# Kernel tuning notes

Hardware: AMD Instinct MI355X
Metric: run time of the kernel (lower is better)

Reference implementation:

```python
import jax, jax.numpy as jnp
import numpy as np

N, E, C, NE, G, T = 20000, 320000, 32, 10, 64, 1000
NB, HID, LAYERS = 8, 64, 2
R_MAX, P_CUT, AVG_NEIGH = 5.0, 6, 16.0
LM = 16  # (max_ell+1)^2 spherical-harmonic components
L_OF_LM = jnp.array([0,1,1,1,2,2,2,2,2,3,3,3,3,3,3,3])


def sph_harm(u):
    # component-normalized real spherical harmonics up to l=3 on unit vectors u [E,3]
    x, y, z = u[:, 0], u[:, 1], u[:, 2]
    s3, s15, s5, s105, s7 = 3**0.5, 15**0.5, 5**0.5, 105**0.5, 7**0.5
    s35_8, s21_8 = (35.0/8.0)**0.5, (21.0/8.0)**0.5
    comps = [jnp.ones_like(x),
             s3*x, s3*y, s3*z,
             s15*x*y, s15*y*z, 0.5*s5*(3*z*z-1.0), s15*x*z, 0.5*s15*(x*x-y*y),
             s35_8*y*(3*x*x-y*y), s105*x*y*z, s21_8*y*(5*z*z-1.0),
             0.5*s7*(5*z*z*z-3*z), s21_8*x*(5*z*z-1.0),
             0.5*s105*z*(x*x-y*y), s35_8*x*(x*x-3*y*y)]
    return jnp.stack(comps, axis=-1)  # [E,16]


def radial_embed(r):
    # Bessel basis with polynomial cutoff (MACE RadialEmbeddingBlock)
    n = jnp.arange(1, NB + 1, dtype=r.dtype)
    rc = jnp.maximum(r, 1e-9)
    bessel = (2.0/R_MAX)**0.5 * jnp.sin(n[None, :]*jnp.pi*rc[:, None]/R_MAX) / rc[:, None]
    xr = r / R_MAX
    p = float(P_CUT)
    f = (1.0 - 0.5*(p+1)*(p+2)*xr**p + p*(p+2)*xr**(p+1) - 0.5*p*(p+1)*xr**(p+2))
    f = f * (xr < 1.0)
    return bessel * f[:, None]  # [E,NB]


def setup_inputs():
    key = jax.random.key(0)
    ks = jax.random.split(key, 16)
    positions = jax.random.normal(ks[0], (N, 3)) * 3.0
    species = jax.random.randint(ks[1], (N,), 0, NE)
    node_attrs = jax.nn.one_hot(species, NE, dtype=jnp.float32)
    edge_index = jax.random.randint(ks[2], (2, E), 0, N)
    shifts = jnp.zeros((E, 3), jnp.float32)
    batch = jnp.sort(jax.random.randint(ks[3], (N,), 0, G))
    t = jax.random.randint(ks[4], (G,), 0, T)
    eps = jax.random.normal(ks[5], (N, NE + 3))
    betas = jnp.linspace(1e-4, 0.02, T)
    alpha_bar = jnp.cumprod(1.0 - betas)
    sc = 0.1
    W_embed = sc * jax.random.normal(ks[6], (NE + 1, C))
    W_r1 = sc * jax.random.normal(ks[7], (LAYERS, NB, HID))
    W_r2 = sc * jax.random.normal(ks[8], (LAYERS, HID, C * 4))
    W_mix = sc * jax.random.normal(ks[9], (LAYERS, 4, C, C))
    W_sc = sc * jax.random.normal(ks[10], (NE, C))
    W_prod = sc * jax.random.normal(ks[11], (LAYERS, 3, C))
    W_ro_s = sc * jax.random.normal(ks[12], (LAYERS, C, NE))
    W_ro_v = sc * jax.random.normal(ks[13], (LAYERS, C))
    return {"positions": positions, "node_attrs": node_attrs, "shifts": shifts,
            "eps": eps, "alpha_bar": alpha_bar, "W_embed": W_embed, "W_r1": W_r1,
            "W_r2": W_r2, "W_mix": W_mix, "W_sc": W_sc, "W_prod": W_prod,
            "W_ro_s": W_ro_s, "W_ro_v": W_ro_v, "edge_index": edge_index,
            "batch": batch, "t": t}


def reference(positions, node_attrs, shifts, eps, alpha_bar, W_embed, W_r1, W_r2,
              W_mix, W_sc, W_prod, W_ro_s, W_ro_v, edge_index, batch, t):
    sender, receiver = edge_index[0], edge_index[1]
    # diffusion: noise positions and attrs (DDPM q(x_t|x_0))
    ab = alpha_bar[t][batch][:, None]                       # [N,1]
    attrs0 = node_attrs / 4.0
    pos_noisy = jnp.sqrt(ab) * positions + jnp.sqrt(1.0 - ab) * eps[:, -3:]
    attrs_noisy = jnp.sqrt(ab) * attrs0 + jnp.sqrt(1.0 - ab) * eps[:, :NE]
    tf = (t.astype(jnp.float32) / T)[batch][:, None]
    h = jnp.concatenate([attrs_noisy, tf], axis=-1) @ W_embed  # [N,C]
    # edge geometry
    vec = pos_noisy[receiver] - pos_noisy[sender] + shifts
    r = jnp.sqrt(jnp.sum(vec * vec, axis=-1) + 1e-12)
    Y = sph_harm(vec / r[:, None])                          # [E,16]
    ef = radial_embed(r)                                    # [E,NB]
    scalar = h
    pred = jnp.zeros((N, NE + 3), h.dtype)
    for layer in range(LAYERS):
        rw = jax.nn.silu(ef @ W_r1[layer]) @ W_r2[layer]    # [E,4C]
        rw = rw.reshape(E, C, 4)[:, :, L_OF_LM]             # [E,C,16]
        msg = rw * scalar[sender][:, :, None] * Y[:, None, :]
        agg = jax.ops.segment_sum(msg, receiver, num_segments=N) / AVG_NEIGH
        Wm = W_mix[layer][L_OF_LM]                          # [16,C,C]
        feats = jnp.einsum('nck,kcd->ndk', agg, Wm)         # per-l channel mix
        s = feats[:, :, 0]
        poly = W_prod[layer, 0] + W_prod[layer, 1] * s + W_prod[layer, 2] * s * s
        feats = feats * poly[:, :, None]                    # correlation-3 product
        if layer == 0:
            feats = feats.at[:, :, 0].add(attrs_noisy @ W_sc)  # element skip
        scalar = feats[:, :, 0]
        pred_s = scalar @ W_ro_s[layer]                     # [N,NE]
        pred_v = jnp.einsum('ncm,c->nm', feats[:, :, 1:4], W_ro_v[layer])  # [N,3]
        pred = pred + jnp.concatenate([pred_s, pred_v], axis=-1)
    err = (pred - eps) ** 2
    loss_pos = jax.ops.segment_sum(err[:, -3:].sum(-1), batch, num_segments=G)
    loss_lab = jax.ops.segment_sum(err[:, :NE].sum(-1), batch, num_segments=G)
    nn = jax.ops.segment_sum(jnp.ones((N,), pred.dtype), batch, num_segments=G)
    loss = 0.5 * (loss_pos + loss_lab) / (jnp.maximum(nn, 1.0) * (3 + NE))
    return loss
```

## Files before the change

### kernel.cpp

```cpp
#include <hip/hip_runtime.h>

typedef unsigned short ushort_t;
typedef unsigned int uint_t;

#define NN 20000
#define EE 320000
#define CC 32
#define NEL 10
#define GG 64
#define TTT 1000
#define NBB 8
#define HIDD 64
#define EPB 256

typedef __attribute__((ext_vector_type(8))) short bf16x8;
typedef __attribute__((ext_vector_type(4))) float f32x4;

__device__ __forceinline__ float bits2f(uint_t b) { union { uint_t u; float f; } v; v.u = b; return v.f; }
__device__ __forceinline__ ushort_t f2b(float f) {
  union { float f; uint_t u; } v; v.f = f;
  uint_t r = (v.u + 0x7fffu + ((v.u >> 16) & 1u)) >> 16;
  return (ushort_t)r;
}
__device__ __forceinline__ uint_t pk(float a, float b) {
  return (uint_t)f2b(a) | ((uint_t)f2b(b) << 16);
}
__device__ __forceinline__ float lo16(uint_t u) { return bits2f(u << 16); }
__device__ __forceinline__ float hi16(uint_t u) { return bits2f(u & 0xffff0000u); }

__global__ __launch_bounds__(256) void k_prep(
    const float* __restrict__ positions, const float* __restrict__ node_attrs,
    const float* __restrict__ eps, const float* __restrict__ alpha_bar,
    const float* __restrict__ W_embed, const float* __restrict__ W_sc,
    const int* __restrict__ batch, const int* __restrict__ tarr,
    float* __restrict__ pos_noisy, float* __restrict__ scalA,
    float* __restrict__ sc_skip, float* __restrict__ pred, int* __restrict__ deg)
{
  int n = blockIdx.x * 256 + threadIdx.x;
  if (n >= NN) return;
  deg[n] = 0;
  int g = batch[n];
  int tn = tarr[g];
  float ab = alpha_bar[tn];
  float sa = sqrtf(ab), sb = sqrtf(fmaxf(1.0f - ab, 0.0f));
#pragma unroll
  for (int j = 0; j < 3; ++j)
    pos_noisy[n * 3 + j] = sa * positions[n * 3 + j] + sb * eps[n * 13 + 10 + j];
  float an[10];
#pragma unroll
  for (int j = 0; j < 10; ++j)
    an[j] = sa * 0.25f * node_attrs[n * 10 + j] + sb * eps[n * 13 + j];
  float tf = (float)tn * (1.0f / (float)TTT);
  for (int d = 0; d < CC; ++d) {
    float h = tf * W_embed[10 * CC + d];
    float sk = 0.0f;
#pragma unroll
    for (int j = 0; j < 10; ++j) {
      h = fmaf(an[j], W_embed[j * CC + d], h);
      sk = fmaf(an[j], W_sc[j * CC + d], sk);
    }
    scalA[n * CC + d] = h;
    sc_skip[n * CC + d] = sk;
  }
#pragma unroll
  for (int j = 0; j < 13; ++j) pred[n * 13 + j] = 0.0f;
}

__global__ __launch_bounds__(256) void k_edge_deg(const int* __restrict__ ei,
    int* __restrict__ deg)
{
  int e = blockIdx.x * 256 + threadIdx.x;
  atomicAdd(&deg[ei[EE + e]], 1);
}

__global__ __launch_bounds__(1024) void k_scan(const int* __restrict__ deg,
    int* __restrict__ offs, int* __restrict__ cursor,
    float* __restrict__ lnum, float* __restrict__ lcnt)
{
  __shared__ int wsums[16];
  __shared__ int woffs[16];
  int tid = threadIdx.x, lane = tid & 63, wv = tid >> 6;
  if (tid < GG) { lnum[tid] = 0.0f; lcnt[tid] = 0.0f; }
  int base = tid * 20;
  int loc[20];
  int s = 0;
#pragma unroll
  for (int j = 0; j < 20; ++j) {
    int idx = base + j;
    int v = (idx < NN) ? deg[idx] : 0;
    loc[j] = s; s += v;
  }
  int inc = s;
  for (int o = 1; o < 64; o <<= 1) {
    int v = __shfl_up(inc, o, 64);
    if (lane >= o) inc += v;
  }
  if (lane == 63) wsums[wv] = inc;
  __syncthreads();
  if (wv == 0 && lane < 16) {
    int v = wsums[lane];
    int i2 = v;
    for (int o = 1; o < 16; o <<= 1) {
      int vv = __shfl_up(i2, o, 16);
      if (lane >= o) i2 += vv;
    }
    woffs[lane] = i2 - v;
  }
  __syncthreads();
  int texcl = woffs[wv] + (inc - s);
#pragma unroll
  for (int j = 0; j < 20; ++j) {
    int idx = base + j;
    if (idx < NN) { int v = texcl + loc[j]; offs[idx] = v; cursor[idx] = v; }
  }
  if (tid == 1023) offs[NN] = EE;
}

__global__ __launch_bounds__(256) void k_edge2(
    const float* __restrict__ pos_noisy, const float* __restrict__ shifts,
    const int* __restrict__ ei, int* __restrict__ cursor,
    ushort_t* __restrict__ Ys, ushort_t* __restrict__ efs, int* __restrict__ snds)
{
  int e = blockIdx.x * 256 + threadIdx.x;
  int snd = ei[e], rcv = ei[EE + e];
  float vx = pos_noisy[rcv * 3 + 0] - pos_noisy[snd * 3 + 0] + shifts[e * 3 + 0];
  float vy = pos_noisy[rcv * 3 + 1] - pos_noisy[snd * 3 + 1] + shifts[e * 3 + 1];
  float vz = pos_noisy[rcv * 3 + 2] - pos_noisy[snd * 3 + 2] + shifts[e * 3 + 2];
  float r2 = vx * vx + vy * vy + vz * vz + 1e-12f;
  float r = sqrtf(r2);
  float inv = 1.0f / r;
  float x = vx * inv, y = vy * inv, z = vz * inv;

  const float s3 = 1.7320508075688772f, s15 = 3.872983346207417f, s5 = 2.23606797749979f;
  const float s105 = 10.246950765959598f, s7 = 2.6457513110645907f;
  const float s35_8 = 2.091650066335189f, s21_8 = 1.6201851746019651f;
  float yv[16];
  yv[0] = 1.0f;
  yv[1] = s3 * x; yv[2] = s3 * y; yv[3] = s3 * z;
  yv[4] = s15 * x * y;
  yv[5] = s15 * y * z;
  yv[6] = 0.5f * s5 * (3.0f * z * z - 1.0f);
  yv[7] = s15 * x * z;
  yv[8] = 0.5f * s15 * (x * x - y * y);
  yv[9] = s35_8 * y * (3.0f * x * x - y * y);
  yv[10] = s105 * x * y * z;
  yv[11] = s21_8 * y * (5.0f * z * z - 1.0f);
  yv[12] = 0.5f * s7 * (5.0f * z * z * z - 3.0f * z);
  yv[13] = s21_8 * x * (5.0f * z * z - 1.0f);
  yv[14] = 0.5f * s105 * z * (x * x - y * y);
  yv[15] = s35_8 * x * (x * x - 3.0f * y * y);

  float rc = fmaxf(r, 1e-9f);
  float pref = 0.6324555320336759f / rc;
  float th = 0.6283185307179586f * rc;
  float s1 = __sinf(th), c1 = __cosf(th);
  float xr = r * 0.2f;
  float fcut = 0.0f;
  if (xr < 1.0f) {
    float x2 = xr * xr, x3 = x2 * xr;
    float x6 = x3 * x3, x7 = x6 * xr, x8 = x7 * xr;
    fcut = 1.0f - 28.0f * x6 + 48.0f * x7 - 21.0f * x8;
  }
  float efv[8];
  float sp = 0.0f, scur = s1, c2 = 2.0f * c1;
#pragma unroll
  for (int b = 0; b < 8; ++b) {
    efv[b] = pref * scur * fcut;
    float nx = c2 * scur - sp;
    sp = scur; scur = nx;
  }

  int slot = atomicAdd(&cursor[rcv], 1);
  snds[slot] = snd;
  uint4* Y4 = (uint4*)Ys;
  Y4[(size_t)slot * 2 + 0] = make_uint4(pk(yv[0], yv[1]), pk(yv[2], yv[3]),
                                        pk(yv[4], yv[5]), pk(yv[6], yv[7]));
  Y4[(size_t)slot * 2 + 1] = make_uint4(pk(yv[8], yv[9]), pk(yv[10], yv[11]),
                                        pk(yv[12], yv[13]), pk(yv[14], yv[15]));
  ((uint4*)efs)[slot] = make_uint4(pk(efv[0], efv[1]), pk(efv[2], efv[3]),
                                   pk(efv[4], efv[5]), pk(efv[6], efv[7]));
}

__global__ __launch_bounds__(256) void k_rw_mfma(
    const ushort_t* __restrict__ efs, const float* __restrict__ W_r1,
    const float* __restrict__ W_r2, ushort_t* __restrict__ rwc, int layer)
{
  __shared__ __align__(16) ushort_t w2t[128][72];
  __shared__ __align__(16) ushort_t h1[EPB][72];
  int tid = threadIdx.x;
  const float* W1g = W_r1 + layer * NBB * HIDD;
  const float* W2g = W_r2 + layer * HIDD * 128;
  for (int idx = tid; idx < HIDD * 128; idx += 256) {
    int k = idx >> 7, n = idx & 127;
    w2t[n][k] = f2b(W2g[idx]);
  }
  {
    int e = blockIdx.x * EPB + tid;
    uint4 q = ((const uint4*)efs)[e];
    float efr[8] = {lo16(q.x), hi16(q.x), lo16(q.y), hi16(q.y),
                    lo16(q.z), hi16(q.z), lo16(q.w), hi16(q.w)};
    for (int hc = 0; hc < 8; ++hc) {
      float v[8];
#pragma unroll
      for (int hh = 0; hh < 8; ++hh) {
        int h = hc * 8 + hh;
        float t = 0.0f;
#pragma unroll
        for (int b = 0; b < 8; ++b) t = fmaf(efr[b], W1g[b * HIDD + h], t);
        v[hh] = t / (1.0f + __expf(-t));
      }
      *(uint4*)&h1[tid][hc * 8] = make_uint4(pk(v[0], v[1]), pk(v[2], v[3]),
                                             pk(v[4], v[5]), pk(v[6], v[7]));
    }
  }
  __syncthreads();
  int w = tid >> 6, lane = tid & 63;
  int c = lane & 15, quad = lane >> 4;
  bf16x8 bfr[16];
#pragma unroll
  for (int nt = 0; nt < 8; ++nt)
#pragma unroll
    for (int kt = 0; kt < 2; ++kt)
      bfr[nt * 2 + kt] = *(const bf16x8*)&w2t[nt * 16 + c][kt * 32 + quad * 8];
  int mb0 = w * 64;
#pragma unroll
  for (int mt = 0; mt < 4; ++mt) {
    int mbase = mb0 + mt * 16;
    bf16x8 a0 = *(const bf16x8*)&h1[mbase + c][quad * 8];
    bf16x8 a1 = *(const bf16x8*)&h1[mbase + c][32 + quad * 8];
    size_t erow = (size_t)blockIdx.x * EPB + mbase + quad * 4;
#pragma unroll
    for (int nt = 0; nt < 8; ++nt) {
      f32x4 acc = {0.0f, 0.0f, 0.0f, 0.0f};
      acc = __builtin_amdgcn_mfma_f32_16x16x32_bf16(a0, bfr[nt * 2 + 0], acc, 0, 0, 0);
      acc = __builtin_amdgcn_mfma_f32_16x16x32_bf16(a1, bfr[nt * 2 + 1], acc, 0, 0, 0);
      int col = nt * 16 + c;
#pragma unroll
      for (int r = 0; r < 4; ++r)
        rwc[(erow + r) * 128 + col] = f2b(acc[r]);
    }
  }
}

__global__ __launch_bounds__(256) void k_layer(
    const ushort_t* __restrict__ Ys, const ushort_t* __restrict__ rwc,
    const int* __restrict__ snds,
    const float* __restrict__ scal_in, float* __restrict__ scal_out,
    const int* __restrict__ offs,
    const float* __restrict__ W_mix, const float* __restrict__ W_prod,
    const float* __restrict__ W_ro_s, const float* __restrict__ W_ro_v,
    const float* __restrict__ sc_skip, float* __restrict__ pred, int layer)
{
  __shared__ float lagg[4][CC][16];
  __shared__ float lf[4][CC][4];
  int w = threadIdx.x >> 6, lane = threadIdx.x & 63;
  int n = blockIdx.x * 4 + w;
  int c = lane >> 1;
  int kh = lane & 1;
  int kb = kh * 8;
  int i0 = offs[n], i1 = offs[n + 1];
  float acc0 = 0, acc1 = 0, acc2 = 0, acc3 = 0, acc4 = 0, acc5 = 0, acc6 = 0, acc7 = 0;
  const uint4* Y4 = (const uint4*)Ys;
  const uint2* rw2 = (const uint2*)rwc;
  for (int s = i0; s < i1; ++s) {
    uint4 q = Y4[(size_t)s * 2 + kh];
    uint2 rp = rw2[(size_t)s * 32 + c];
    float ss = scal_in[snds[s] * CC + c];
    float r0 = lo16(rp.x), r1 = hi16(rp.x), r2v = lo16(rp.y), r3 = hi16(rp.y);
    float w0 = kh ? r2v : r0;
    float w13 = kh ? r3 : r1;
    float w47 = kh ? r3 : r2v;
    float ya0 = lo16(q.x), ya1 = hi16(q.x), ya2 = lo16(q.y), ya3 = hi16(q.y);
    float yb0 = lo16(q.z), yb1 = hi16(q.z), yb2 = lo16(q.w), yb3 = hi16(q.w);
    acc0 = fmaf(w0 * ss, ya0, acc0);
    acc1 = fmaf(w13 * ss, ya1, acc1);
    acc2 = fmaf(w13 * ss, ya2, acc2);
    acc3 = fmaf(w13 * ss, ya3, acc3);
    acc4 = fmaf(w47 * ss, yb0, acc4);
    acc5 = fmaf(w47 * ss, yb1, acc5);
    acc6 = fmaf(w47 * ss, yb2, acc6);
    acc7 = fmaf(w47 * ss, yb3, acc7);
  }
  const float invavg = 1.0f / 16.0f;
  lagg[w][c][kb + 0] = acc0 * invavg;
  lagg[w][c][kb + 1] = acc1 * invavg;
  lagg[w][c][kb + 2] = acc2 * invavg;
  lagg[w][c][kb + 3] = acc3 * invavg;
  lagg[w][c][kb + 4] = acc4 * invavg;
  lagg[w][c][kb + 5] = acc5 * invavg;
  lagg[w][c][kb + 6] = acc6 * invavg;
  lagg[w][c][kb + 7] = acc7 * invavg;
  __syncthreads();
  int d = c;
  float ft[8] = {0, 0, 0, 0, 0, 0, 0, 0};
  const float* Wm = W_mix + layer * 4096;
  for (int cc2 = 0; cc2 < CC; ++cc2) {
    float m0 = Wm[cc2 * CC + d];
    float m1 = Wm[1024 + cc2 * CC + d];
    float m2 = Wm[2048 + cc2 * CC + d];
    float m3 = Wm[3072 + cc2 * CC + d];
    float u0 = kh ? m2 : m0;
    float u13 = kh ? m3 : m1;
    float u47 = kh ? m3 : m2;
    ft[0] = fmaf(lagg[w][cc2][kb + 0], u0, ft[0]);
    ft[1] = fmaf(lagg[w][cc2][kb + 1], u13, ft[1]);
    ft[2] = fmaf(lagg[w][cc2][kb + 2], u13, ft[2]);
    ft[3] = fmaf(lagg[w][cc2][kb + 3], u13, ft[3]);
    ft[4] = fmaf(lagg[w][cc2][kb + 4], u47, ft[4]);
    ft[5] = fmaf(lagg[w][cc2][kb + 5], u47, ft[5]);
    ft[6] = fmaf(lagg[w][cc2][kb + 6], u47, ft[6]);
    ft[7] = fmaf(lagg[w][cc2][kb + 7], u47, ft[7]);
  }
  float s = __shfl(ft[0], lane & 62, 64);
  const float* Wp = W_prod + layer * 96;
  float p0 = Wp[d], p1 = Wp[32 + d], p2 = Wp[64 + d];
  float poly = fmaf(fmaf(p2, s, p1), s, p0);
#pragma unroll
  for (int j = 0; j < 8; ++j) ft[j] *= poly;
  if (layer == 0 && kh == 0) ft[0] += sc_skip[n * CC + d];
  if (kh == 0) {
    scal_out[n * CC + d] = ft[0];
    lf[w][d][0] = ft[0]; lf[w][d][1] = ft[1]; lf[w][d][2] = ft[2]; lf[w][d][3] = ft[3];
  }
  __syncthreads();
  if (lane < 13) {
    float sum = 0.0f;
    if (lane < 10) {
      const float* Wr = W_ro_s + layer * CC * NEL;
      for (int dd = 0; dd < CC; ++dd) sum = fmaf(lf[w][dd][0], Wr[dd * NEL + lane], sum);
    } else {
      int mm = lane - 10;
      const float* Wv = W_ro_v + layer * CC;
      for (int dd = 0; dd < CC; ++dd) sum = fmaf(lf[w][dd][1 + mm], Wv[dd], sum);
    }
    pred[n * 13 + lane] += sum;
  }
}

__global__ __launch_bounds__(256) void k_loss(const float* __restrict__ pred,
    const float* __restrict__ eps, const int* __restrict__ batch,
    float* __restrict__ lnum, float* __restrict__ lcnt)
{
  __shared__ float psum[GG];
  __shared__ int pcnt[GG];
  int tid = threadIdx.x;
  if (tid < GG) { psum[tid] = 0.0f; pcnt[tid] = 0; }
  __syncthreads();
  int n = blockIdx.x * 256 + tid;
  if (n < NN) {
    int g = batch[n];
    float sum = 0.0f;
#pragma unroll
    for (int j = 0; j < 13; ++j) {
      float dlt = pred[n * 13 + j] - eps[n * 13 + j];
      sum = fmaf(dlt, dlt, sum);
    }
    atomicAdd(&psum[g], sum);
    atomicAdd(&pcnt[g], 1);
  }
  __syncthreads();
  if (tid < GG && pcnt[tid] > 0) {
    atomicAdd(&lnum[tid], psum[tid]);
    atomicAdd(&lcnt[tid], (float)pcnt[tid]);
  }
}

__global__ void k_final(const float* __restrict__ lnum, const float* __restrict__ lcnt,
    float* __restrict__ out)
{
  int g = threadIdx.x;
  if (g < GG) {
    float nn = fmaxf(lcnt[g], 1.0f);
    out[g] = 0.5f * lnum[g] / (nn * 13.0f);
  }
}

extern "C" void kernel_launch(void* const* d_in, const int* in_sizes, int n_in,
                              void* d_out, int out_size, void* d_ws, size_t ws_size,
                              hipStream_t stream) {
  const float* positions  = (const float*)d_in[0];
  const float* node_attrs = (const float*)d_in[1];
  const float* shifts     = (const float*)d_in[2];
  const float* eps        = (const float*)d_in[3];
  const float* alpha_bar  = (const float*)d_in[4];
  const float* W_embed    = (const float*)d_in[5];
  const float* W_r1       = (const float*)d_in[6];
  const float* W_r2       = (const float*)d_in[7];
  const float* W_mix      = (const float*)d_in[8];
  const float* W_sc       = (const float*)d_in[9];
  const float* W_prod     = (const float*)d_in[10];
  const float* W_ro_s     = (const float*)d_in[11];
  const float* W_ro_v     = (const float*)d_in[12];
  const int* edge_index   = (const int*)d_in[13];
  const int* batch        = (const int*)d_in[14];
  const int* tarr         = (const int*)d_in[15];
  float* out = (float*)d_out;

  char* ws = (char*)d_ws;
  size_t off = 0;
  auto alloc = [&](size_t bytes) -> void* {
    void* p = ws + off;
    off = (off + bytes + 255) & ~(size_t)255;
    return p;
  };
  float* pos_noisy = (float*)alloc(NN * 3 * 4);
  float* scalA     = (float*)alloc(NN * CC * 4);
  float* scalB     = (float*)alloc(NN * CC * 4);
  float* sc_skip   = (float*)alloc(NN * CC * 4);
  float* pred      = (float*)alloc(NN * 13 * 4);
  ushort_t* Ys     = (ushort_t*)alloc((size_t)EE * 16 * 2);
  ushort_t* efs    = (ushort_t*)alloc((size_t)EE * 8 * 2);
  int* snds        = (int*)alloc((size_t)EE * 4);
  ushort_t* rwc    = (ushort_t*)alloc((size_t)EE * 128 * 2);
  int* deg         = (int*)alloc(NN * 4);
  int* offs        = (int*)alloc((NN + 1) * 4);
  int* cursor      = (int*)alloc(NN * 4);
  float* lnum      = (float*)alloc(GG * 4);
  float* lcnt      = (float*)alloc(GG * 4);
  (void)ws_size; (void)in_sizes; (void)n_in; (void)out_size;

  const int NB_N = (NN + 255) / 256;
  const int NB_E = EE / 256;

  k_prep<<<NB_N, 256, 0, stream>>>(positions, node_attrs, eps, alpha_bar, W_embed,
                                   W_sc, batch, tarr, pos_noisy, scalA, sc_skip, pred, deg);
  k_edge_deg<<<NB_E, 256, 0, stream>>>(edge_index, deg);
  k_scan<<<1, 1024, 0, stream>>>(deg, offs, cursor, lnum, lcnt);
  k_edge2<<<NB_E, 256, 0, stream>>>(pos_noisy, shifts, edge_index, cursor, Ys, efs, snds);

  for (int layer = 0; layer < 2; ++layer) {
    const float* sin_p = (layer == 0) ? scalA : scalB;
    float* sout_p      = (layer == 0) ? scalB : scalA;
    k_rw_mfma<<<NB_E, 256, 0, stream>>>(efs, W_r1, W_r2, rwc, layer);
    k_layer<<<NN / 4, 256, 0, stream>>>(Ys, rwc, snds, sin_p, sout_p, offs,
                                        W_mix, W_prod, W_ro_s, W_ro_v,
                                        sc_skip, pred, layer);
  }

  k_loss<<<NB_N, 256, 0, stream>>>(pred, eps, batch, lnum, lcnt);
  k_final<<<1, 64, 0, stream>>>(lnum, lcnt, out);
}
```

Baseline: 362.4 us.

## Fold sender scalar gather into radial-weight MFMA kernel; unroll edge loop by two

The multiplication by the sender node's scalar features moves out of the per-node aggregation loop and into the radial-weight MFMA epilogue, so rwc already holds the weight times the sender scalar. This removes the dependent snds load followed by the scal_in gather from the latency-bound aggregation loop, which is also unrolled by two to keep more loads in flight. In exchange the MFMA kernel now performs scattered gathers from scal_in in its epilogue, and the product is rounded to bf16 before storage, which changes precision slightly.

```diff
diff --git a/kernel.cpp b/kernel.cpp
--- a/kernel.cpp
+++ b/kernel.cpp
@@ -183,7 +183,8 @@
 
 __global__ __launch_bounds__(256) void k_rw_mfma(
     const ushort_t* __restrict__ efs, const float* __restrict__ W_r1,
-    const float* __restrict__ W_r2, ushort_t* __restrict__ rwc, int layer)
+    const float* __restrict__ W_r2, const int* __restrict__ snds,
+    const float* __restrict__ scal_in, ushort_t* __restrict__ rwc, int layer)
 {
   __shared__ __align__(16) ushort_t w2t[128][72];
   __shared__ __align__(16) ushort_t h1[EPB][72];
@@ -229,23 +230,29 @@
     bf16x8 a0 = *(const bf16x8*)&h1[mbase + c][quad * 8];
     bf16x8 a1 = *(const bf16x8*)&h1[mbase + c][32 + quad * 8];
     size_t erow = (size_t)blockIdx.x * EPB + mbase + quad * 4;
+    int4 sn = *(const int4*)&snds[erow];
+    const float* sb0 = scal_in + (size_t)sn.x * CC;
+    const float* sb1 = scal_in + (size_t)sn.y * CC;
+    const float* sb2 = scal_in + (size_t)sn.z * CC;
+    const float* sb3 = scal_in + (size_t)sn.w * CC;
 #pragma unroll
     for (int nt = 0; nt < 8; ++nt) {
       f32x4 acc = {0.0f, 0.0f, 0.0f, 0.0f};
       acc = __builtin_amdgcn_mfma_f32_16x16x32_bf16(a0, bfr[nt * 2 + 0], acc, 0, 0, 0);
       acc = __builtin_amdgcn_mfma_f32_16x16x32_bf16(a1, bfr[nt * 2 + 1], acc, 0, 0, 0);
       int col = nt * 16 + c;
-#pragma unroll
-      for (int r = 0; r < 4; ++r)
-        rwc[(erow + r) * 128 + col] = f2b(acc[r]);
+      int cc = col >> 2;
+      rwc[(erow + 0) * 128 + col] = f2b(acc[0] * sb0[cc]);
+      rwc[(erow + 1) * 128 + col] = f2b(acc[1] * sb1[cc]);
+      rwc[(erow + 2) * 128 + col] = f2b(acc[2] * sb2[cc]);
+      rwc[(erow + 3) * 128 + col] = f2b(acc[3] * sb3[cc]);
     }
   }
 }
 
 __global__ __launch_bounds__(256) void k_layer(
     const ushort_t* __restrict__ Ys, const ushort_t* __restrict__ rwc,
-    const int* __restrict__ snds,
-    const float* __restrict__ scal_in, float* __restrict__ scal_out,
+    float* __restrict__ scal_out,
     const int* __restrict__ offs,
     const float* __restrict__ W_mix, const float* __restrict__ W_prod,
     const float* __restrict__ W_ro_s, const float* __restrict__ W_ro_v,
@@ -262,24 +269,50 @@
   float acc0 = 0, acc1 = 0, acc2 = 0, acc3 = 0, acc4 = 0, acc5 = 0, acc6 = 0, acc7 = 0;
   const uint4* Y4 = (const uint4*)Ys;
   const uint2* rw2 = (const uint2*)rwc;
-  for (int s = i0; s < i1; ++s) {
+  int s = i0;
+  for (; s + 2 <= i1; s += 2) {
+    uint4 qa = Y4[(size_t)s * 2 + kh];
+    uint2 ra = rw2[(size_t)s * 32 + c];
+    uint4 qb = Y4[(size_t)(s + 1) * 2 + kh];
+    uint2 rb = rw2[(size_t)(s + 1) * 32 + c];
+    {
+      float r0 = lo16(ra.x), r1 = hi16(ra.x), r2v = lo16(ra.y), r3 = hi16(ra.y);
+      float w0 = kh ? r2v : r0, w13 = kh ? r3 : r1, w47 = kh ? r3 : r2v;
+      acc0 = fmaf(w0,  lo16(qa.x), acc0);
+      acc1 = fmaf(w13, hi16(qa.x), acc1);
+      acc2 = fmaf(w13, lo16(qa.y), acc2);
+      acc3 = fmaf(w13, hi16(qa.y), acc3);
+      acc4 = fmaf(w47, lo16(qa.z), acc4);
+      acc5 = fmaf(w47, hi16(qa.z), acc5);
+      acc6 = fmaf(w47, lo16(qa.w), acc6);
+      acc7 = fmaf(w47, hi16(qa.w), acc7);
+    }
+    {
+      float r0 = lo16(rb.x), r1 = hi16(rb.x), r2v = lo16(rb.y), r3 = hi16(rb.y);
+      float w0 = kh ? r2v : r0, w13 = kh ? r3 : r1, w47 = kh ? r3 : r2v;
+      acc0 = fmaf(w0,  lo16(qb.x), acc0);
+      acc1 = fmaf(w13, hi16(qb.x), acc1);
+      acc2 = fmaf(w13, lo16(qb.y), acc2);
+      acc3 = fmaf(w13, hi16(qb.y), acc3);
+      acc4 = fmaf(w47, lo16(qb.z), acc4);
+      acc5 = fmaf(w47, hi16(qb.z), acc5);
+      acc6 = fmaf(w47, lo16(qb.w), acc6);
+      acc7 = fmaf(w47, hi16(qb.w), acc7);
+    }
+  }
+  if (s < i1) {
     uint4 q = Y4[(size_t)s * 2 + kh];
     uint2 rp = rw2[(size_t)s * 32 + c];
-    float ss = scal_in[snds[s] * CC + c];
     float r0 = lo16(rp.x), r1 = hi16(rp.x), r2v = lo16(rp.y), r3 = hi16(rp.y);
-    float w0 = kh ? r2v : r0;
-    float w13 = kh ? r3 : r1;
-    float w47 = kh ? r3 : r2v;
-    float ya0 = lo16(q.x), ya1 = hi16(q.x), ya2 = lo16(q.y), ya3 = hi16(q.y);
-    float yb0 = lo16(q.z), yb1 = hi16(q.z), yb2 = lo16(q.w), yb3 = hi16(q.w);
-    acc0 = fmaf(w0 * ss, ya0, acc0);
-    acc1 = fmaf(w13 * ss, ya1, acc1);
-    acc2 = fmaf(w13 * ss, ya2, acc2);
-    acc3 = fmaf(w13 * ss, ya3, acc3);
-    acc4 = fmaf(w47 * ss, yb0, acc4);
-    acc5 = fmaf(w47 * ss, yb1, acc5);
-    acc6 = fmaf(w47 * ss, yb2, acc6);
-    acc7 = fmaf(w47 * ss, yb3, acc7);
+    float w0 = kh ? r2v : r0, w13 = kh ? r3 : r1, w47 = kh ? r3 : r2v;
+    acc0 = fmaf(w0,  lo16(q.x), acc0);
+    acc1 = fmaf(w13, hi16(q.x), acc1);
+    acc2 = fmaf(w13, lo16(q.y), acc2);
+    acc3 = fmaf(w13, hi16(q.y), acc3);
+    acc4 = fmaf(w47, lo16(q.z), acc4);
+    acc5 = fmaf(w47, hi16(q.z), acc5);
+    acc6 = fmaf(w47, lo16(q.w), acc6);
+    acc7 = fmaf(w47, hi16(q.w), acc7);
   }
   const float invavg = 1.0f / 16.0f;
   lagg[w][c][kb + 0] = acc0 * invavg;
@@ -311,10 +344,10 @@
     ft[6] = fmaf(lagg[w][cc2][kb + 6], u47, ft[6]);
     ft[7] = fmaf(lagg[w][cc2][kb + 7], u47, ft[7]);
   }
-  float s = __shfl(ft[0], lane & 62, 64);
+  float sv = __shfl(ft[0], lane & 62, 64);
   const float* Wp = W_prod + layer * 96;
   float p0 = Wp[d], p1 = Wp[32 + d], p2 = Wp[64 + d];
-  float poly = fmaf(fmaf(p2, s, p1), s, p0);
+  float poly = fmaf(fmaf(p2, sv, p1), sv, p0);
 #pragma unroll
   for (int j = 0; j < 8; ++j) ft[j] *= poly;
   if (layer == 0 && kh == 0) ft[0] += sc_skip[n * CC + d];
@@ -431,8 +464,8 @@
   for (int layer = 0; layer < 2; ++layer) {
     const float* sin_p = (layer == 0) ? scalA : scalB;
     float* sout_p      = (layer == 0) ? scalB : scalA;
-    k_rw_mfma<<<NB_E, 256, 0, stream>>>(efs, W_r1, W_r2, rwc, layer);
-    k_layer<<<NN / 4, 256, 0, stream>>>(Ys, rwc, snds, sin_p, sout_p, offs,
+    k_rw_mfma<<<NB_E, 256, 0, stream>>>(efs, W_r1, W_r2, snds, sin_p, rwc, layer);
+    k_layer<<<NN / 4, 256, 0, stream>>>(Ys, rwc, sout_p, offs,
                                         W_mix, W_prod, W_ro_s, W_ro_v,
                                         sc_skip, pred, layer);
   }
```

Result: faster. 341.6 us (-5.7%).

## Fuse radial MLP MFMA into per-node message aggregation kernel

Applied to the files above, without the earlier changes.

The radial-weight MFMA kernel and the per-node layer kernel are merged into one. Each block handles 4 receiver nodes: it computes the radial MLP for their edges in 16-edge tiles, multiplies by sender scalars and spherical harmonics, and reduces into shared memory with atomics. This removes the large bf16 per-edge weight buffer that was written and then read back every layer, plus one launch per layer. In exchange each block re-converts W_r2 into shared memory, wave work becomes uneven across nodes, and degree is capped at 64 edges per node, which would silently drop edges for higher-degree nodes.

```diff
diff --git a/kernel.cpp b/kernel.cpp
--- a/kernel.cpp
+++ b/kernel.cpp
@@ -11,7 +11,8 @@
 #define TTT 1000
 #define NBB 8
 #define HIDD 64
-#define EPB 256
+#define NPB 4
+#define MAXDEG 64
 
 typedef __attribute__((ext_vector_type(8))) short bf16x8;
 typedef __attribute__((ext_vector_type(4))) float f32x4;
@@ -27,6 +28,7 @@
 }
 __device__ __forceinline__ float lo16(uint_t u) { return bits2f(u << 16); }
 __device__ __forceinline__ float hi16(uint_t u) { return bits2f(u & 0xffff0000u); }
+__device__ __forceinline__ float b2f(ushort_t u) { return bits2f(((uint_t)u) << 16); }
 
 __global__ __launch_bounds__(256) void k_prep(
     const float* __restrict__ positions, const float* __restrict__ node_attrs,
@@ -181,149 +183,195 @@
                                    pk(efv[4], efv[5]), pk(efv[6], efv[7]));
 }
 
-__global__ __launch_bounds__(256) void k_rw_mfma(
-    const ushort_t* __restrict__ efs, const float* __restrict__ W_r1,
-    const float* __restrict__ W_r2, ushort_t* __restrict__ rwc, int layer)
+__global__ __launch_bounds__(256) void k_fused(
+    const ushort_t* __restrict__ efs, const ushort_t* __restrict__ Ys,
+    const int* __restrict__ snds, const int* __restrict__ offs,
+    const float* __restrict__ W_r1, const float* __restrict__ W_r2,
+    const float* __restrict__ scal_in, float* __restrict__ scal_out,
+    const float* __restrict__ W_mix, const float* __restrict__ W_prod,
+    const float* __restrict__ W_ro_s, const float* __restrict__ W_ro_v,
+    const float* __restrict__ sc_skip, float* __restrict__ pred, int layer)
 {
   __shared__ __align__(16) ushort_t w2t[128][72];
-  __shared__ __align__(16) ushort_t h1[EPB][72];
+  __shared__ __align__(16) ushort_t ysh[256][16];
+  __shared__ float agg[NPB][CC][20];
+  __shared__ float lf[NPB][CC][4];
+
   int tid = threadIdx.x;
+  int n0 = blockIdx.x * NPB;
   const float* W1g = W_r1 + layer * NBB * HIDD;
   const float* W2g = W_r2 + layer * HIDD * 128;
+
+  int o0 = offs[n0], o1 = offs[n0 + 1], o2 = offs[n0 + 2], o3 = offs[n0 + 3], o4 = offs[n0 + 4];
+  int d0 = min(o1 - o0, MAXDEG), d1 = min(o2 - o1, MAXDEG);
+  int d2 = min(o3 - o2, MAXDEG), d3 = min(o4 - o3, MAXDEG);
+  int p1 = (d0 + 15) >> 4;
+  int p2 = p1 + ((d1 + 15) >> 4);
+  int p3 = p2 + ((d2 + 15) >> 4);
+  int T  = p3 + ((d3 + 15) >> 4);
+
+  for (int i = tid; i < NPB * CC * 20; i += 256) ((float*)agg)[i] = 0.0f;
   for (int idx = tid; idx < HIDD * 128; idx += 256) {
     int k = idx >> 7, n = idx & 127;
     w2t[n][k] = f2b(W2g[idx]);
   }
-  {
-    int e = blockIdx.x * EPB + tid;
-    uint4 q = ((const uint4*)efs)[e];
-    float efr[8] = {lo16(q.x), hi16(q.x), lo16(q.y), hi16(q.y),
-                    lo16(q.z), hi16(q.z), lo16(q.w), hi16(q.w)};
-    for (int hc = 0; hc < 8; ++hc) {
-      float v[8];
-#pragma unroll
-      for (int hh = 0; hh < 8; ++hh) {
-        int h = hc * 8 + hh;
-        float t = 0.0f;
-#pragma unroll
-        for (int b = 0; b < 8; ++b) t = fmaf(efr[b], W1g[b * HIDD + h], t);
-        v[hh] = t / (1.0f + __expf(-t));
-      }
-      *(uint4*)&h1[tid][hc * 8] = make_uint4(pk(v[0], v[1]), pk(v[2], v[3]),
-                                             pk(v[4], v[5]), pk(v[6], v[7]));
-    }
-  }
-  __syncthreads();
+  if (tid < T * 16) {
+    int t = tid >> 4, r = tid & 15;
+    int j = (t < p1) ? 0 : (t < p2) ? 1 : (t < p3) ? 2 : 3;
+    int oj = (j == 0) ? o0 : (j == 1) ? o1 : (j == 2) ? o2 : o3;
+    int pj = (j == 0) ? 0 : (j == 1) ? p1 : (j == 2) ? p2 : p3;
+    int dj = (j == 0) ? d0 : (j == 1) ? d1 : (j == 2) ? d2 : d3;
+    int k = (t - pj) * 16 + r;
+    uint4 a = make_uint4(0, 0, 0, 0), b = make_uint4(0, 0, 0, 0);
+    if (k < dj) {
+      const uint4* Y4 = (const uint4*)Ys;
+      size_t ge = (size_t)(oj + k);
+      a = Y4[ge * 2]; b = Y4[ge * 2 + 1];
+    }
+    *(uint4*)&ysh[tid][0] = a;
+    *(uint4*)&ysh[tid][8] = b;
+  }
+  __syncthreads();
+
   int w = tid >> 6, lane = tid & 63;
   int c = lane & 15, quad = lane >> 4;
-  bf16x8 bfr[16];
-#pragma unroll
-  for (int nt = 0; nt < 8; ++nt)
-#pragma unroll
-    for (int kt = 0; kt < 2; ++kt)
-      bfr[nt * 2 + kt] = *(const bf16x8*)&w2t[nt * 16 + c][kt * 32 + quad * 8];
-  int mb0 = w * 64;
-#pragma unroll
-  for (int mt = 0; mt < 4; ++mt) {
-    int mbase = mb0 + mt * 16;
-    bf16x8 a0 = *(const bf16x8*)&h1[mbase + c][quad * 8];
-    bf16x8 a1 = *(const bf16x8*)&h1[mbase + c][32 + quad * 8];
-    size_t erow = (size_t)blockIdx.x * EPB + mbase + quad * 4;
+  int l = c & 3, nlm = 2 * l + 1, lmb = l * l;
+
+  for (int t = w; t < T; t += 4) {
+    int j = (t < p1) ? 0 : (t < p2) ? 1 : (t < p3) ? 2 : 3;
+    int oj = (j == 0) ? o0 : (j == 1) ? o1 : (j == 2) ? o2 : o3;
+    int pj = (j == 0) ? 0 : (j == 1) ? p1 : (j == 2) ? p2 : p3;
+    int dj = (j == 0) ? d0 : (j == 1) ? d1 : (j == 2) ? d2 : d3;
+    int kbase = (t - pj) * 16;
+
+    bf16x8 a0, a1;
+    {
+      int kc = kbase + c;
+      float ef8[8] = {0, 0, 0, 0, 0, 0, 0, 0};
+      if (kc < dj) {
+        uint4 q = ((const uint4*)efs)[(size_t)(oj + kc)];
+        ef8[0] = lo16(q.x); ef8[1] = hi16(q.x); ef8[2] = lo16(q.y); ef8[3] = hi16(q.y);
+        ef8[4] = lo16(q.z); ef8[5] = hi16(q.z); ef8[6] = lo16(q.w); ef8[7] = hi16(q.w);
+      }
+      float h0[8] = {0, 0, 0, 0, 0, 0, 0, 0};
+      float h1v[8] = {0, 0, 0, 0, 0, 0, 0, 0};
+#pragma unroll
+      for (int b = 0; b < 8; ++b) {
+        const float* Wb = W1g + b * HIDD;
+        float4 wa = *(const float4*)&Wb[quad * 8];
+        float4 wbv = *(const float4*)&Wb[quad * 8 + 4];
+        float4 wc = *(const float4*)&Wb[32 + quad * 8];
+        float4 wd = *(const float4*)&Wb[32 + quad * 8 + 4];
+        float e = ef8[b];
+        h0[0] = fmaf(e, wa.x, h0[0]); h0[1] = fmaf(e, wa.y, h0[1]);
+        h0[2] = fmaf(e, wa.z, h0[2]); h0[3] = fmaf(e, wa.w, h0[3]);
+        h0[4] = fmaf(e, wbv.x, h0[4]); h0[5] = fmaf(e, wbv.y, h0[5]);
+        h0[6] = fmaf(e, wbv.z, h0[6]); h0[7] = fmaf(e, wbv.w, h0[7]);
+        h1v[0] = fmaf(e, wc.x, h1v[0]); h1v[1] = fmaf(e, wc.y, h1v[1]);
+        h1v[2] = fmaf(e, wc.z, h1v[2]); h1v[3] = fmaf(e, wc.w, h1v[3]);
+        h1v[4] = fmaf(e, wd.x, h1v[4]); h1v[5] = fmaf(e, wd.y, h1v[5]);
+        h1v[6] = fmaf(e, wd.z, h1v[6]); h1v[7] = fmaf(e, wd.w, h1v[7]);
+      }
+#pragma unroll
+      for (int jj = 0; jj < 8; ++jj) {
+        float v0 = h0[jj];  v0 = v0 / (1.0f + __expf(-v0));
+        float v1 = h1v[jj]; v1 = v1 / (1.0f + __expf(-v1));
+        a0[jj] = (short)f2b(v0);
+        a1[jj] = (short)f2b(v1);
+      }
+    }
+
+    int snd_[4];
+#pragma unroll
+    for (int r = 0; r < 4; ++r) {
+      int kr = kbase + quad * 4 + r;
+      int ger = oj + ((kr < dj) ? kr : 0);
+      snd_[r] = snds[ger];
+    }
+    float yv_[4][7];
+#pragma unroll
+    for (int r = 0; r < 4; ++r) {
+      int slot = t * 16 + quad * 4 + r;
+#pragma unroll
+      for (int i = 0; i < 7; ++i)
+        if (i < nlm) yv_[r][i] = b2f(ysh[slot][lmb + i]);
+    }
+
 #pragma unroll
     for (int nt = 0; nt < 8; ++nt) {
+      bf16x8 b0 = *(const bf16x8*)&w2t[nt * 16 + c][quad * 8];
+      bf16x8 b1 = *(const bf16x8*)&w2t[nt * 16 + c][32 + quad * 8];
       f32x4 acc = {0.0f, 0.0f, 0.0f, 0.0f};
-      acc = __builtin_amdgcn_mfma_f32_16x16x32_bf16(a0, bfr[nt * 2 + 0], acc, 0, 0, 0);
-      acc = __builtin_amdgcn_mfma_f32_16x16x32_bf16(a1, bfr[nt * 2 + 1], acc, 0, 0, 0);
-      int col = nt * 16 + c;
-#pragma unroll
-      for (int r = 0; r < 4; ++r)
-        rwc[(erow + r) * 128 + col] = f2b(acc[r]);
-    }
-  }
-}
-
-__global__ __launch_bounds__(256) void k_layer(
-    const ushort_t* __restrict__ Ys, const ushort_t* __restrict__ rwc,
-    const int* __restrict__ snds,
-    const float* __restrict__ scal_in, float* __restrict__ scal_out,
-    const int* __restrict__ offs,
-    const float* __restrict__ W_mix, const float* __restrict__ W_prod,
-    const float* __restrict__ W_ro_s, const float* __restrict__ W_ro_v,
-    const float* __restrict__ sc_skip, float* __restrict__ pred, int layer)
-{
-  __shared__ float lagg[4][CC][16];
-  __shared__ float lf[4][CC][4];
-  int w = threadIdx.x >> 6, lane = threadIdx.x & 63;
-  int n = blockIdx.x * 4 + w;
-  int c = lane >> 1;
-  int kh = lane & 1;
-  int kb = kh * 8;
-  int i0 = offs[n], i1 = offs[n + 1];
-  float acc0 = 0, acc1 = 0, acc2 = 0, acc3 = 0, acc4 = 0, acc5 = 0, acc6 = 0, acc7 = 0;
-  const uint4* Y4 = (const uint4*)Ys;
-  const uint2* rw2 = (const uint2*)rwc;
-  for (int s = i0; s < i1; ++s) {
-    uint4 q = Y4[(size_t)s * 2 + kh];
-    uint2 rp = rw2[(size_t)s * 32 + c];
-    float ss = scal_in[snds[s] * CC + c];
-    float r0 = lo16(rp.x), r1 = hi16(rp.x), r2v = lo16(rp.y), r3 = hi16(rp.y);
-    float w0 = kh ? r2v : r0;
-    float w13 = kh ? r3 : r1;
-    float w47 = kh ? r3 : r2v;
-    float ya0 = lo16(q.x), ya1 = hi16(q.x), ya2 = lo16(q.y), ya3 = hi16(q.y);
-    float yb0 = lo16(q.z), yb1 = hi16(q.z), yb2 = lo16(q.w), yb3 = hi16(q.w);
-    acc0 = fmaf(w0 * ss, ya0, acc0);
-    acc1 = fmaf(w13 * ss, ya1, acc1);
-    acc2 = fmaf(w13 * ss, ya2, acc2);
-    acc3 = fmaf(w13 * ss, ya3, acc3);
-    acc4 = fmaf(w47 * ss, yb0, acc4);
-    acc5 = fmaf(w47 * ss, yb1, acc5);
-    acc6 = fmaf(w47 * ss, yb2, acc6);
-    acc7 = fmaf(w47 * ss, yb3, acc7);
-  }
-  const float invavg = 1.0f / 16.0f;
-  lagg[w][c][kb + 0] = acc0 * invavg;
-  lagg[w][c][kb + 1] = acc1 * invavg;
-  lagg[w][c][kb + 2] = acc2 * invavg;
-  lagg[w][c][kb + 3] = acc3 * invavg;
-  lagg[w][c][kb + 4] = acc4 * invavg;
-  lagg[w][c][kb + 5] = acc5 * invavg;
-  lagg[w][c][kb + 6] = acc6 * invavg;
-  lagg[w][c][kb + 7] = acc7 * invavg;
-  __syncthreads();
-  int d = c;
-  float ft[8] = {0, 0, 0, 0, 0, 0, 0, 0};
-  const float* Wm = W_mix + layer * 4096;
-  for (int cc2 = 0; cc2 < CC; ++cc2) {
-    float m0 = Wm[cc2 * CC + d];
-    float m1 = Wm[1024 + cc2 * CC + d];
-    float m2 = Wm[2048 + cc2 * CC + d];
-    float m3 = Wm[3072 + cc2 * CC + d];
-    float u0 = kh ? m2 : m0;
-    float u13 = kh ? m3 : m1;
-    float u47 = kh ? m3 : m2;
-    ft[0] = fmaf(lagg[w][cc2][kb + 0], u0, ft[0]);
-    ft[1] = fmaf(lagg[w][cc2][kb + 1], u13, ft[1]);
-    ft[2] = fmaf(lagg[w][cc2][kb + 2], u13, ft[2]);
-    ft[3] = fmaf(lagg[w][cc2][kb + 3], u13, ft[3]);
-    ft[4] = fmaf(lagg[w][cc2][kb + 4], u47, ft[4]);
-    ft[5] = fmaf(lagg[w][cc2][kb + 5], u47, ft[5]);
-    ft[6] = fmaf(lagg[w][cc2][kb + 6], u47, ft[6]);
-    ft[7] = fmaf(lagg[w][cc2][kb + 7], u47, ft[7]);
-  }
-  float s = __shfl(ft[0], lane & 62, 64);
-  const float* Wp = W_prod + layer * 96;
-  float p0 = Wp[d], p1 = Wp[32 + d], p2 = Wp[64 + d];
-  float poly = fmaf(fmaf(p2, s, p1), s, p0);
-#pragma unroll
-  for (int j = 0; j < 8; ++j) ft[j] *= poly;
-  if (layer == 0 && kh == 0) ft[0] += sc_skip[n * CC + d];
-  if (kh == 0) {
-    scal_out[n * CC + d] = ft[0];
-    lf[w][d][0] = ft[0]; lf[w][d][1] = ft[1]; lf[w][d][2] = ft[2]; lf[w][d][3] = ft[3];
-  }
-  __syncthreads();
+      acc = __builtin_amdgcn_mfma_f32_16x16x32_bf16(a0, b0, acc, 0, 0, 0);
+      acc = __builtin_amdgcn_mfma_f32_16x16x32_bf16(a1, b1, acc, 0, 0, 0);
+      int cc = 4 * nt + (c >> 2);
+      float v[7];
+#pragma unroll
+      for (int i = 0; i < 7; ++i) v[i] = 0.0f;
+#pragma unroll
+      for (int r = 0; r < 4; ++r) {
+        float val = acc[r] * scal_in[(size_t)snd_[r] * CC + cc];
+#pragma unroll
+        for (int i = 0; i < 7; ++i)
+          if (i < nlm) v[i] = fmaf(val, yv_[r][i], v[i]);
+      }
+#pragma unroll
+      for (int i = 0; i < 7; ++i) {
+        if (i < nlm) {
+          float s2 = v[i];
+          s2 += __shfl_xor(s2, 16, 64);
+          s2 += __shfl_xor(s2, 32, 64);
+          if (quad == 0) atomicAdd(&agg[j][cc][lmb + i], s2);
+        }
+      }
+    }
+  }
+  __syncthreads();
+
+  {
+    int d = lane >> 1;
+    int kh = lane & 1, kb = kh * 8;
+    int n = n0 + w;
+    float ft[8] = {0, 0, 0, 0, 0, 0, 0, 0};
+    const float* Wm = W_mix + layer * 4096;
+    for (int cc2 = 0; cc2 < CC; ++cc2) {
+      float la[8];
+      *(float4*)&la[0] = *(const float4*)&agg[w][cc2][kb];
+      *(float4*)&la[4] = *(const float4*)&agg[w][cc2][kb + 4];
+      float m0 = Wm[cc2 * CC + d];
+      float m1 = Wm[1024 + cc2 * CC + d];
+      float m2 = Wm[2048 + cc2 * CC + d];
+      float m3 = Wm[3072 + cc2 * CC + d];
+      float u0 = kh ? m2 : m0;
+      float u13 = kh ? m3 : m1;
+      float u47 = kh ? m3 : m2;
+      ft[0] = fmaf(la[0], u0, ft[0]);
+      ft[1] = fmaf(la[1], u13, ft[1]);
+      ft[2] = fmaf(la[2], u13, ft[2]);
+      ft[3] = fmaf(la[3], u13, ft[3]);
+      ft[4] = fmaf(la[4], u47, ft[4]);
+      ft[5] = fmaf(la[5], u47, ft[5]);
+      ft[6] = fmaf(la[6], u47, ft[6]);
+      ft[7] = fmaf(la[7], u47, ft[7]);
+    }
+#pragma unroll
+    for (int i = 0; i < 8; ++i) ft[i] *= (1.0f / 16.0f);
+    float sv = __shfl(ft[0], lane & 62, 64);
+    const float* Wp = W_prod + layer * 96;
+    float p0 = Wp[d], p1v = Wp[32 + d], p2v = Wp[64 + d];
+    float poly = fmaf(fmaf(p2v, sv, p1v), sv, p0);
+#pragma unroll
+    for (int i = 0; i < 8; ++i) ft[i] *= poly;
+    if (layer == 0 && kh == 0) ft[0] += sc_skip[n * CC + d];
+    if (kh == 0) {
+      scal_out[n * CC + d] = ft[0];
+      lf[w][d][0] = ft[0]; lf[w][d][1] = ft[1]; lf[w][d][2] = ft[2]; lf[w][d][3] = ft[3];
+    }
+  }
+  __syncthreads();
+
   if (lane < 13) {
+    int n = n0 + w;
     float sum = 0.0f;
     if (lane < 10) {
       const float* Wr = W_ro_s + layer * CC * NEL;
@@ -411,7 +459,6 @@
   ushort_t* Ys     = (ushort_t*)alloc((size_t)EE * 16 * 2);
   ushort_t* efs    = (ushort_t*)alloc((size_t)EE * 8 * 2);
   int* snds        = (int*)alloc((size_t)EE * 4);
-  ushort_t* rwc    = (ushort_t*)alloc((size_t)EE * 128 * 2);
   int* deg         = (int*)alloc(NN * 4);
   int* offs        = (int*)alloc((NN + 1) * 4);
   int* cursor      = (int*)alloc(NN * 4);
@@ -431,10 +478,9 @@
   for (int layer = 0; layer < 2; ++layer) {
     const float* sin_p = (layer == 0) ? scalA : scalB;
     float* sout_p      = (layer == 0) ? scalB : scalA;
-    k_rw_mfma<<<NB_E, 256, 0, stream>>>(efs, W_r1, W_r2, rwc, layer);
-    k_layer<<<NN / 4, 256, 0, stream>>>(Ys, rwc, snds, sin_p, sout_p, offs,
-                                        W_mix, W_prod, W_ro_s, W_ro_v,
-                                        sc_skip, pred, layer);
+    k_fused<<<NN / NPB, 256, 0, stream>>>(efs, Ys, snds, offs, W_r1, W_r2,
+                                          sin_p, sout_p, W_mix, W_prod,
+                                          W_ro_s, W_ro_v, sc_skip, pred, layer);
   }
 
   k_loss<<<NB_N, 256, 0, stream>>>(pred, eps, batch, lnum, lcnt);
```

Measured after the change: 1.119 ms. 3.09x slower.
